# Performance work log

Hardware: AMD Instinct MI355X
Metric: run time of the kernel (lower is better)

## Reference

```python
import jax, jax.numpy as jnp
import numpy as np

B, N, D, H, DH, F, L, LC = 32, 256, 512, 8, 64, 2048, 8, 2
NEG = -1e9
SCALE = 1.0 / float(np.sqrt(DH))


def _ln(x, g, b, eps=1e-3):
    # keras LayerNormalization default epsilon=1e-3
    m = jnp.mean(x, -1, keepdims=True)
    v = jnp.mean((x - m) ** 2, -1, keepdims=True)
    return (x - m) * jax.lax.rsqrt(v + eps) * g + b


def setup_inputs() -> dict:
    key = jax.random.key(0)
    ks = jax.random.split(key, 20)
    n = lambda k, s: jax.random.normal(k, s, dtype=jnp.float32) * 0.02
    lengths = jax.random.randint(ks[0], (B,), N // 2, N + 1)
    mask = jnp.arange(N)[None, :] < lengths[:, None]  # [B,N] bool
    return {
        'x': jax.random.normal(ks[1], (B, N, D), dtype=jnp.float32),
        'interaction': jax.random.normal(ks[2], (B, N, N, H), dtype=jnp.float32) * 0.1,
        'class_token': n(ks[3], (1, 1, D)),
        'p_ln1_g': jnp.ones((L, D)), 'p_ln1_b': jnp.zeros((L, D)),
        'p_wq': n(ks[4], (L, D, D)), 'p_wk': n(ks[5], (L, D, D)),
        'p_wv': n(ks[6], (L, D, D)), 'p_wo': n(ks[7], (L, D, D)),
        'p_ln2_g': jnp.ones((L, D)), 'p_ln2_b': jnp.zeros((L, D)),
        'p_w1': n(ks[8], (L, D, F)), 'p_b1': jnp.zeros((L, F)),
        'p_w2': n(ks[9], (L, F, D)), 'p_b2': jnp.zeros((L, D)),
        'c_ln1_g': jnp.ones((LC, D)), 'c_ln1_b': jnp.zeros((LC, D)),
        'c_qk': n(ks[10], (LC, D, H, DH)), 'c_qb': jnp.zeros((LC, H, DH)),
        'c_kk': n(ks[11], (LC, D, H, DH)), 'c_kb': jnp.zeros((LC, H, DH)),
        'c_vk': n(ks[12], (LC, D, H, DH)), 'c_vb': jnp.zeros((LC, H, DH)),
        'c_ok': n(ks[13], (LC, H, DH, D)), 'c_ob': jnp.zeros((LC, D)),
        'c_ln2_g': jnp.ones((LC, D)), 'c_ln2_b': jnp.zeros((LC, D)),
        'c_w1': n(ks[14], (LC, D, F)), 'c_b1': jnp.zeros((LC, F)),
        'c_w2': n(ks[15], (LC, F, D)), 'c_b2': jnp.zeros((LC, D)),
        'mask': mask,
    }


def _part_forward(x, interaction, class_token, p_ln1_g, p_ln1_b, p_wq, p_wk, p_wv, p_wo,
                  p_ln2_g, p_ln2_b, p_w1, p_b1, p_w2, p_b2,
                  c_ln1_g, c_ln1_b, c_qk, c_qb, c_kk, c_kb, c_vk, c_vb, c_ok, c_ob,
                  c_ln2_g, c_ln2_b, c_w1, c_b1, c_w2, c_b2, mask):
    # pairwise particle mask [B,1,N,N]; keras Softmax adds (1-mask)*-1e9
    pmask = (mask[:, None, None, :] & mask[:, None, :, None]).astype(x.dtype)
    padd = (1.0 - pmask) * NEG
    inter = jnp.transpose(interaction, (0, 3, 1, 2))  # [B,H,N,N]
    h = x
    for i in range(L):
        # pre-LN interaction self-attention (dropout inactive at inference)
        hn = _ln(h, p_ln1_g[i], p_ln1_b[i])
        q = (hn @ p_wq[i]).reshape(B, N, H, DH)
        k = (hn @ p_wk[i]).reshape(B, N, H, DH)
        v = (hn @ p_wv[i]).reshape(B, N, H, DH)
        s = jnp.einsum('bqhd,bkhd->bhqk', q, k) * SCALE + inter + padd
        a = jax.nn.softmax(s, axis=-1)
        o = jnp.einsum('bhqk,bkhd->bqhd', a, v).reshape(B, N, D) @ p_wo[i]
        h = h + o
        # pre-LN FFN, gelu (exact, tf.nn.gelu default)
        fn = _ln(h, p_ln2_g[i], p_ln2_b[i])
        h = h + (jax.nn.gelu(fn @ p_w1[i] + p_b1[i], approximate=False) @ p_w2[i] + p_b2[i])
    query = jnp.broadcast_to(class_token, (B, 1, D)).astype(x.dtype)
    cmask = jnp.concatenate([jnp.ones((B, 1), bool), mask], axis=1)[:, None, None, :].astype(x.dtype)
    cadd = (1.0 - cmask) * NEG  # [B,1,1,N+1]
    for i in range(LC):
        # class-attention: K/V from LN(concat([token, particles])), Q from RAW token (as in source)
        cat = jnp.concatenate([query, h], axis=1)  # [B,N+1,D]
        cn = _ln(cat, c_ln1_g[i], c_ln1_b[i])
        qh = jnp.einsum('bqd,dhk->bqhk', query, c_qk[i]) + c_qb[i]
        kh = jnp.einsum('bsd,dhk->bshk', cn, c_kk[i]) + c_kb[i]
        vh = jnp.einsum('bsd,dhk->bshk', cn, c_vk[i]) + c_vb[i]
        s = jnp.einsum('bqhk,bshk->bhqs', qh, kh) * SCALE + cadd
        a = jax.nn.softmax(s, axis=-1)
        o = jnp.einsum('bhqs,bshk->bqhk', a, vh)
        o = jnp.einsum('bqhk,hkd->bqd', o, c_ok[i]) + c_ob[i]
        query = query + o
        fn = _ln(query, c_ln2_g[i], c_ln2_b[i])
        query = query + (jax.nn.gelu(fn @ c_w1[i] + c_b1[i], approximate=False) @ c_w2[i] + c_b2[i])
    return query  # [B,1,D]


def reference(x, interaction, class_token, p_ln1_g, p_ln1_b, p_wq, p_wk, p_wv, p_wo,
              p_ln2_g, p_ln2_b, p_w1, p_b1, p_w2, p_b2,
              c_ln1_g, c_ln1_b, c_qk, c_qb, c_kk, c_kb, c_vk, c_vb, c_ok, c_ob,
              c_ln2_g, c_ln2_b, c_w1, c_b1, c_w2, c_b2, mask):
    return _part_forward(x, interaction, class_token, p_ln1_g, p_ln1_b, p_wq, p_wk, p_wv, p_wo,
                         p_ln2_g, p_ln2_b, p_w1, p_b1, p_w2, p_b2,
                         c_ln1_g, c_ln1_b, c_qk, c_qb, c_kk, c_kb, c_vk, c_vb, c_ok, c_ob,
                         c_ln2_g, c_ln2_b, c_w1, c_b1, c_w2, c_b2, mask)
```

## Files before the change

### kernel.cpp

```cpp
#include <hip/hip_runtime.h>
#include <hip/hip_fp16.h>

#define B_ 32
#define N_ 256
#define D_ 512
#define H_ 8
#define DH_ 64
#define F_ 2048
#define L_ 8
#define LC_ 2
#define NEG_ (-1e9f)
#define SCALE_ 0.125f
#define LDSK 72
#define KCH_ 128

typedef unsigned short u16;
typedef unsigned int u32;
typedef long long s64;
typedef __attribute__((ext_vector_type(8))) short bf16x8;
typedef __attribute__((ext_vector_type(8))) unsigned short u16x8;
typedef __attribute__((ext_vector_type(4))) float f32x4;

__device__ __forceinline__ float b2f(u16 u) {
    union { u32 i; float f; } v; v.i = ((u32)u) << 16; return v.f;
}
__device__ __forceinline__ u16 f2b(float f) {
    union { float f; u32 i; } v; v.f = f;
    u32 x = v.i;
    u32 r = (x + 0x7FFFu + ((x >> 16) & 1u)) >> 16;
    return (u16)r;
}
__device__ __forceinline__ float h2f(u16 u) {
    __half_raw hr; hr.x = u;
    return __half2float(__half(hr));
}
__device__ __forceinline__ void gld16(u16* lds, const u16* g) {
    __builtin_amdgcn_global_load_lds(
        (const __attribute__((address_space(1))) u16*)g,
        (__attribute__((address_space(3))) u16*)lds, 16, 0, 0);
}
__device__ __forceinline__ float ldf(const void* p, size_t i, int fl) {
    if (fl == 1) return ((const float*)p)[i];
    if (fl == 0) return b2f(((const u16*)p)[i]);
    return h2f(((const u16*)p)[i]);
}
__device__ __forceinline__ void ld4(const void* p, size_t i, int fl, float o[4]) {
    if (fl == 1) {
        const float4 v = *(const float4*)((const float*)p + i);
        o[0] = v.x; o[1] = v.y; o[2] = v.z; o[3] = v.w;
    } else if (fl == 0) {
        const ushort4 v = *(const ushort4*)((const u16*)p + i);
        o[0] = b2f(v.x); o[1] = b2f(v.y); o[2] = b2f(v.z); o[3] = b2f(v.w);
    } else {
        const ushort4 v = *(const ushort4*)((const u16*)p + i);
        o[0] = h2f(v.x); o[1] = h2f(v.y); o[2] = h2f(v.z); o[3] = h2f(v.w);
    }
}

__global__ void sniff_kernel(const u32* __restrict__ g1, int* __restrict__ flag) {
    if (threadIdx.x == 0 && blockIdx.x == 0) {
        u32 w = g1[0];
        int f = 0;
        if (w == 0x3F800000u) f = 1;
        else if (w == 0x3C003C00u) f = 2;
        flag[0] = f;
    }
}

__global__ void mask_decode_kernel(const unsigned char* __restrict__ raw,
                                   float* __restrict__ mf) {
    int i = blockIdx.x * 256 + threadIdx.x;
    if (i >= B_ * N_) return;
    unsigned char c0 = raw[0], c1 = raw[1], c4 = raw[4];
    bool v;
    if (c1 == 0x3F || c1 == 0x3C) {
        v = ((const u16*)raw)[i] != 0;
    } else if (c0 == 1 && c1 == 1) {
        v = raw[i] != 0;
    } else if (c0 == 1 && c1 == 0) {
        if (c4 == 1) v = ((const int*)raw)[i] != 0;
        else v = ((const long long*)raw)[i] != 0;
    } else {
        v = ((const float*)raw)[i] != 0.0f;
    }
    mf[i] = v ? 1.0f : 0.0f;
}

__global__ void cvt_in_kernel(const void* __restrict__ in, float* __restrict__ out,
                              int n, const int* __restrict__ fl) {
    int i = blockIdx.x * 256 + threadIdx.x;
    if (i < n) out[i] = ldf(in, (size_t)i, fl[0]);
}
__global__ void bcast_token_kernel(const void* __restrict__ ct, float* __restrict__ qry,
                                   const int* __restrict__ fl) {
    int i = blockIdx.x * 256 + threadIdx.x;
    qry[i] = ldf(ct, (size_t)(i & (D_ - 1)), fl[0]);
}
__global__ void out_copy_kernel(const float* __restrict__ in, float* __restrict__ out, int n) {
    int i = blockIdx.x * 256 + threadIdx.x;
    if (i < n) out[i] = in[i];
}
__global__ void concat_bias_kernel(const void* __restrict__ b1, s64 o1,
                                   const void* __restrict__ b2, s64 o2,
                                   float* __restrict__ dst, const int* __restrict__ flp) {
    int i = blockIdx.x * 256 + threadIdx.x;
    if (i < 512) dst[i] = ldf(b1, (size_t)(o1 + i), flp[0]);
    else if (i < 1024) dst[i] = ldf(b2, (size_t)(o2 + i - 512), flp[0]);
}

__global__ __launch_bounds__(256) void inter_t_kernel(const void* __restrict__ inter,
                                                      const float* __restrict__ mf,
                                                      u16* __restrict__ out,
                                                      const int* __restrict__ flp) {
    __shared__ float tile[256][9];
    __shared__ float mks[256];
    int fl = flp[0];
    int bq = blockIdx.x;
    int b = bq >> 8, q = bq & 255;
    int t = threadIdx.x;
    size_t base = (size_t)bq * 2048;
#pragma unroll
    for (int p = 0; p < 8; ++p) {
        int e = p * 256 + t;
        tile[e >> 3][e & 7] = ldf(inter, base + e, fl);
    }
    mks[t] = mf[b * 256 + t];
    __syncthreads();
    float mq = mf[b * 256 + q];
    int h = t >> 5;
    int k0 = (t & 31) * 8;
    u16x8 v8;
#pragma unroll
    for (int ii = 0; ii < 8; ++ii) {
        int k = k0 + ii;
        float v = tile[k][h];
        if (mq * mks[k] < 0.5f) v += NEG_;
        v8[ii] = (short)f2b(v);
    }
    *(u16x8*)(out + (((size_t)(b * 8 + h) * 256 + q) * 256 + k0)) = v8;
}

__global__ __launch_bounds__(256) void transpose_w_kernel(const void* __restrict__ W, s64 weoff,
                                                          int Nst, int Kd,
                                                          u16* __restrict__ wt,
                                                          const int* __restrict__ flp) {
    __shared__ float tile[32][33];
    int fl = flp[0];
    int n0 = blockIdx.x * 32, k0 = blockIdx.y * 32;
    int tr = threadIdx.x >> 5, tc = threadIdx.x & 31;
#pragma unroll
    for (int p = 0; p < 4; ++p) {
        int kk = p * 8 + tr;
        tile[kk][tc] = ldf(W, (size_t)(weoff + (s64)(k0 + kk) * Nst + n0 + tc), fl);
    }
    __syncthreads();
#pragma unroll
    for (int p = 0; p < 4; ++p) {
        int nn = p * 8 + tr;
        wt[(s64)(n0 + nn) * Kd + k0 + tc] = f2b(tile[tc][nn]);
    }
}

__global__ __launch_bounds__(256) void twt6_kernel(const void* __restrict__ wq,
                                                   const void* __restrict__ wk,
                                                   const void* __restrict__ wv,
                                                   const void* __restrict__ wo,
                                                   const void* __restrict__ w1,
                                                   const void* __restrict__ w2,
                                                   s64 off44, s64 offw1, s64 offw2,
                                                   u16* __restrict__ wtqkv,
                                                   u16* __restrict__ wto,
                                                   u16* __restrict__ wt1,
                                                   u16* __restrict__ wt2,
                                                   const int* __restrict__ flp) {
    __shared__ float tile[32][33];
    int fl = flp[0];
    int bid = blockIdx.x;
    const void* W; s64 weoff; int Nst, Kd; u16* dst; int lb;
    if (bid < 256)       { W = wq; weoff = off44; Nst = 512;  Kd = 512;  dst = wtqkv;          lb = bid; }
    else if (bid < 512)  { W = wk; weoff = off44; Nst = 512;  Kd = 512;  dst = wtqkv + 262144; lb = bid - 256; }
    else if (bid < 768)  { W = wv; weoff = off44; Nst = 512;  Kd = 512;  dst = wtqkv + 524288; lb = bid - 512; }
    else if (bid < 1024) { W = wo; weoff = off44; Nst = 512;  Kd = 512;  dst = wto;            lb = bid - 768; }
    else if (bid < 2048) { W = w1; weoff = offw1; Nst = 2048; Kd = 512;  dst = wt1;            lb = bid - 1024; }
    else                 { W = w2; weoff = offw2; Nst = 512;  Kd = 2048; dst = wt2;            lb = bid - 2048; }
    int nx = Nst >> 5;
    int n0 = (lb % nx) << 5, k0 = (lb / nx) << 5;
    int tr = threadIdx.x >> 5, tc = threadIdx.x & 31;
#pragma unroll
    for (int p = 0; p < 4; ++p) {
        int kk = p * 8 + tr;
        tile[kk][tc] = ldf(W, (size_t)(weoff + (s64)(k0 + kk) * Nst + n0 + tc), fl);
    }
    __syncthreads();
#pragma unroll
    for (int p = 0; p < 4; ++p) {
        int nn = p * 8 + tr;
        dst[(s64)(n0 + nn) * Kd + k0 + tc] = f2b(tile[tc][nn]);
    }
}

__global__ __launch_bounds__(256) void ln_kernel(const float* __restrict__ in,
                                                 const void* __restrict__ g,
                                                 const void* __restrict__ bta,
                                                 s64 peoff,
                                                 u16* __restrict__ out,
                                                 const int* __restrict__ flp) {
    __shared__ float ws4[4];
    __shared__ float wsq[4];
    int fl = flp[0];
    size_t row = blockIdx.x;
    int t = threadIdx.x;
    float x0 = in[row * D_ + t];
    float x1 = in[row * D_ + 256 + t];
    float s = x0 + x1;
#pragma unroll
    for (int off = 32; off > 0; off >>= 1) s += __shfl_xor(s, off);
    if ((t & 63) == 0) ws4[t >> 6] = s;
    __syncthreads();
    float mean = (ws4[0] + ws4[1] + ws4[2] + ws4[3]) * (1.0f / D_);
    float d0 = x0 - mean, d1 = x1 - mean;
    float sq = d0 * d0 + d1 * d1;
#pragma unroll
    for (int off = 32; off > 0; off >>= 1) sq += __shfl_xor(sq, off);
    if ((t & 63) == 0) wsq[t >> 6] = sq;
    __syncthreads();
    float var = (wsq[0] + wsq[1] + wsq[2] + wsq[3]) * (1.0f / D_);
    float inv = 1.0f / sqrtf(var + 1e-3f);
    out[row * D_ + t]       = f2b(d0 * inv * ldf(g, peoff + t, fl)       + ldf(bta, peoff + t, fl));
    out[row * D_ + 256 + t] = f2b(d1 * inv * ldf(g, peoff + 256 + t, fl) + ldf(bta, peoff + 256 + t, fl));
}

__global__ __launch_bounds__(256) void ln_cat_kernel(const float* __restrict__ qry,
                                                     const float* __restrict__ h,
                                                     const void* __restrict__ g,
                                                     const void* __restrict__ bta,
                                                     s64 peoff,
                                                     u16* __restrict__ out,
                                                     const int* __restrict__ flp) {
    __shared__ float ws4[4];
    __shared__ float wsq[4];
    int fl = flp[0];
    size_t row = blockIdx.x;
    int b = (int)(row / 257);
    int r = (int)(row % 257);
    const float* src = (r == 0) ? (qry + (size_t)b * D_)
                                : (h + ((size_t)b * N_ + (r - 1)) * D_);
    int t = threadIdx.x;
    float x0 = src[t];
    float x1 = src[256 + t];
    float s = x0 + x1;
#pragma unroll
    for (int off = 32; off > 0; off >>= 1) s += __shfl_xor(s, off);
    if ((t & 63) == 0) ws4[t >> 6] = s;
    __syncthreads();
    float mean = (ws4[0] + ws4[1] + ws4[2] + ws4[3]) * (1.0f / D_);
    float d0 = x0 - mean, d1 = x1 - mean;
    float sq = d0 * d0 + d1 * d1;
#pragma unroll
    for (int off = 32; off > 0; off >>= 1) sq += __shfl_xor(sq, off);
    if ((t & 63) == 0) wsq[t >> 6] = sq;
    __syncthreads();
    float var = (wsq[0] + wsq[1] + wsq[2] + wsq[3]) * (1.0f / D_);
    float inv = 1.0f / sqrtf(var + 1e-3f);
    out[row * D_ + t]       = f2b(d0 * inv * ldf(g, peoff + t, fl)       + ldf(bta, peoff + t, fl));
    out[row * D_ + 256 + t] = f2b(d1 * inv * ldf(g, peoff + 256 + t, fl) + ldf(bta, peoff + 256 + t, fl));
}

__global__ __launch_bounds__(512) void mfma_gemm_t(const u16* __restrict__ A,
                                                   const u16* __restrict__ Wt,
                                                   int wst, int wkoff,
                                                   const void* __restrict__ bias, s64 beoff,
                                                   int bflag,
                                                   const float* __restrict__ res,
                                                   void* __restrict__ C, int cbf,
                                                   int M, int N, int K, int act,
                                                   const int* __restrict__ flp) {
    __shared__ u16 Alds[4 * 128 * 32];
    __shared__ u16 Blds[4 * 128 * 32];
    int tid = threadIdx.x;
    int gx = gridDim.x;
    int nwg = gx * gridDim.y;
    int orig = blockIdx.y * gx + blockIdx.x;
    int xcd = orig & 7;
    int qq = nwg >> 3, rr = nwg & 7;
    int wg = (xcd < rr ? xcd * (qq + 1) : rr * (qq + 1) + (xcd - rr) * qq) + (orig >> 3);
    int bx = wg % gx, by = wg / gx;
    int bm = by << 7, bn = bx << 7;
    int wid = tid >> 6, lane = tid & 63;
    int wm = (wid >> 2) << 6, wn = (wid & 3) << 5;
    int l15 = lane & 15, q = lane >> 4;
    f32x4 acc[4][2];
#pragma unroll
    for (int a = 0; a < 4; ++a)
#pragma unroll
        for (int b = 0; b < 2; ++b) acc[a][b] = (f32x4){0.f, 0.f, 0.f, 0.f};
    int srow = tid >> 2;
    int sseg = tid & 3;
    int xseg = sseg ^ (srow & 3);
    int gr = bm + srow; if (gr >= M) gr = M - 1;
    const u16* arow = A + (size_t)gr * K + (xseg << 3);
    const u16* brow = Wt + (size_t)(bn + srow) * wst + wkoff + (xseg << 3);
    int dstoff = srow * 32 + (sseg << 3);
    auto stage = [&](int buf, int k0) {
        gld16(&Alds[buf * 4096 + dstoff], arow + k0);
        gld16(&Blds[buf * 4096 + dstoff], brow + k0);
    };
    int nt = K >> 5;
    stage(0, 0);
    stage(1, 32);
    stage(2, 64);
    int sg = (q ^ (l15 & 3)) << 3;
    for (int t = 0; t < nt; ++t) {
        int rem = nt - 1 - t;
        if (rem >= 2)      asm volatile("s_waitcnt vmcnt(4)" ::: "memory");
        else if (rem == 1) asm volatile("s_waitcnt vmcnt(2)" ::: "memory");
        else               asm volatile("s_waitcnt vmcnt(0)" ::: "memory");
        __builtin_amdgcn_s_barrier();
        __builtin_amdgcn_sched_barrier(0);
        if (t + 3 < nt) stage((t + 3) & 3, (t + 3) << 5);
        const u16* Ac = Alds + (t & 3) * 4096;
        const u16* Bc = Blds + (t & 3) * 4096;
        bf16x8 af[4], bfr[2];
#pragma unroll
        for (int mt = 0; mt < 4; ++mt)
            af[mt] = *(const bf16x8*)(&Ac[(wm + mt * 16 + l15) * 32 + sg]);
#pragma unroll
        for (int nt2 = 0; nt2 < 2; ++nt2)
            bfr[nt2] = *(const bf16x8*)(&Bc[(wn + nt2 * 16 + l15) * 32 + sg]);
#pragma unroll
        for (int mt = 0; mt < 4; ++mt)
#pragma unroll
            for (int nt2 = 0; nt2 < 2; ++nt2)
                acc[mt][nt2] = __builtin_amdgcn_mfma_f32_16x16x32_bf16(
                    af[mt], bfr[nt2], acc[mt][nt2], 0, 0, 0);
        __builtin_amdgcn_sched_barrier(0);
    }
    int fl = (bflag >= 0) ? bflag : flp[0];
#pragma unroll
    for (int nt2 = 0; nt2 < 2; ++nt2) {
        int col = bn + wn + nt2 * 16 + l15;
        float bv = bias ? ldf(bias, (size_t)(beoff + col), fl) : 0.f;
#pragma unroll
        for (int mt = 0; mt < 4; ++mt) {
#pragma unroll
            for (int i = 0; i < 4; ++i) {
                int row = bm + wm + mt * 16 + q * 4 + i;
                if (row >= M) continue;
                float c = acc[mt][nt2][i] + bv;
                if (act) c = 0.5f * c * (1.0f + erff(c * 0.70710678118654752f));
                if (res) c += res[(size_t)row * N + col];
                if (cbf) ((u16*)C)[(size_t)row * N + col] = f2b(c);
                else     ((float*)C)[(size_t)row * N + col] = c;
            }
        }
    }
}

__global__ __launch_bounds__(256) void skinny_gemm_kernel(const void* __restrict__ A, int abf,
                                                          const void* __restrict__ W, s64 weoff,
                                                          int wst,
                                                          float* __restrict__ Cp,
                                                          int N, int K,
                                                          const int* __restrict__ flp) {
    __shared__ float As[32 * KCH_];
    int wfl = flp[0];
    int tid = threadIdx.x;
    int bn = blockIdx.x << 6;
    int ks = blockIdx.y;
    int k0 = ks * KCH_;
#pragma unroll
    for (int p = 0; p < (32 * KCH_) / 1024; ++p) {
        int idx = p * 1024 + tid * 4;
        int m = idx >> 7, c = idx & (KCH_ - 1);
        size_t gi = (size_t)m * K + k0 + c;
        if (abf) {
            const ushort4 v = *(const ushort4*)((const u16*)A + gi);
            As[idx]     = b2f(v.x);
            As[idx + 1] = b2f(v.y);
            As[idx + 2] = b2f(v.z);
            As[idx + 3] = b2f(v.w);
        } else {
            *(float4*)&As[idx] = *(const float4*)((const float*)A + gi);
        }
    }
    __syncthreads();
    int tx = tid & 63, ty = tid >> 6;
    int n = bn + tx;
    float acc[8] = {0.f, 0.f, 0.f, 0.f, 0.f, 0.f, 0.f, 0.f};
#pragma unroll 4
    for (int kk = 0; kk < KCH_; kk += 4) {
        float w0 = ldf(W, (size_t)(weoff + (s64)(k0 + kk) * wst + n), wfl);
        float w1 = ldf(W, (size_t)(weoff + (s64)(k0 + kk + 1) * wst + n), wfl);
        float w2 = ldf(W, (size_t)(weoff + (s64)(k0 + kk + 2) * wst + n), wfl);
        float w3 = ldf(W, (size_t)(weoff + (s64)(k0 + kk + 3) * wst + n), wfl);
#pragma unroll
        for (int r = 0; r < 8; ++r) {
            const float4 a = *(const float4*)&As[(ty * 8 + r) * KCH_ + kk];
            acc[r] += a.x * w0 + a.y * w1 + a.z * w2 + a.w * w3;
        }
    }
#pragma unroll
    for (int r = 0; r < 8; ++r)
        Cp[((size_t)ks * 32 + ty * 8 + r) * N + n] = acc[r];
}

__global__ __launch_bounds__(256) void skinny_epi_kernel(const float* __restrict__ Cp,
                                                         int KS, int N,
                                                         const void* __restrict__ bias, s64 beoff,
                                                         const float* __restrict__ res,
                                                         float* __restrict__ C, int act,
                                                         const int* __restrict__ flp) {
    int i = blockIdx.x * 256 + threadIdx.x;
    if (i >= 32 * N) return;
    int n = i % N;
    float s = 0.f;
    for (int ks = 0; ks < KS; ++ks) s += Cp[(size_t)ks * 32 * N + i];
    if (bias) s += ldf(bias, (size_t)(beoff + n), flp[0]);
    if (act) s = 0.5f * s * (1.0f + erff(s * 0.70710678118654752f));
    if (res) s += res[i];
    C[i] = s;
}

__global__ __launch_bounds__(256) void attn_mfma_kernel(const u16* __restrict__ QKV,
                                                        const u16* __restrict__ IT,
                                                        u16* __restrict__ O) {
    __shared__ u16 KV[256 * 72];
    __shared__ u16 Amat[64 * 264];
    int li = blockIdx.y * 4 + blockIdx.x;
    int slot = li >> 3;
    int bh = (li & 7) * 32 + (slot >> 2);
    int q0 = (slot & 3) << 6;
    int b = bh >> 3, hh = bh & 7;
    int tid = threadIdx.x;
    int w = tid >> 6, l = tid & 63, q2 = l >> 4, l15 = l & 15;
    int qrow = q0 + (w << 4) + l15;
    const u16* qptr = QKV + (size_t)(b * N_ + qrow) * 1536 + hh * DH_ + (q2 << 3);
    bf16x8 aq0 = *(const bf16x8*)(qptr);
    bf16x8 aq1 = *(const bf16x8*)(qptr + 32);
    {
        int r = tid >> 3, seg = (tid & 7) << 3;
#pragma unroll
        for (int p = 0; p < 8; ++p) {
            int k = p * 32 + r;
            *(u16x8*)(&KV[k * LDSK + seg]) =
                *(const u16x8*)(QKV + (size_t)(b * N_ + k) * 1536 + 512 + hh * DH_ + seg);
        }
    }
    u16x8 vreg[8];
    {
        const u16* vptr = QKV + (size_t)(b * N_ + (w << 6)) * 1536 + 1024 + hh * DH_ + l;
#pragma unroll
        for (int s = 0; s < 8; ++s)
#pragma unroll
            for (int e = 0; e < 8; ++e)
                vreg[s][e] = vptr[(size_t)(s * 8 + e) * 1536];
    }
    const u16* itp = IT + ((size_t)bh * N_ + q0 + (w << 4) + (q2 << 2)) * N_ + l15;
    u16 itv0[16], itv1[16], itv2[16], itv3[16];
#pragma unroll
    for (int t = 0; t < 16; ++t) {
        itv0[t] = itp[t * 16];
        itv1[t] = itp[(size_t)N_ + t * 16];
        itv2[t] = itp[(size_t)2 * N_ + t * 16];
        itv3[t] = itp[(size_t)3 * N_ + t * 16];
    }
    asm volatile("s_waitcnt lgkmcnt(0)" ::: "memory");
    __builtin_amdgcn_s_barrier();
    __builtin_amdgcn_sched_barrier(0);
    f32x4 acc[16];
#pragma unroll
    for (int t = 0; t < 16; ++t) {
        const u16* kp = &KV[(t * 16 + l15) * LDSK + (q2 << 3)];
        bf16x8 b0 = *(const bf16x8*)(kp);
        bf16x8 b1 = *(const bf16x8*)(kp + 32);
        f32x4 z = (f32x4){0.f, 0.f, 0.f, 0.f};
        z = __builtin_amdgcn_mfma_f32_16x16x32_bf16(aq0, b0, z, 0, 0, 0);
        acc[t] = __builtin_amdgcn_mfma_f32_16x16x32_bf16(aq1, b1, z, 0, 0, 0);
    }
    asm volatile("s_waitcnt lgkmcnt(0)" ::: "memory");
    __builtin_amdgcn_s_barrier();
    __builtin_amdgcn_sched_barrier(0);
#pragma unroll
    for (int s = 0; s < 8; ++s)
        *(u16x8*)(&KV[l * 264 + (w << 6) + s * 8]) = vreg[s];
    float mx[4] = {-3e38f, -3e38f, -3e38f, -3e38f};
#pragma unroll
    for (int t = 0; t < 16; ++t) {
        float s0 = acc[t][0] * SCALE_ + b2f(itv0[t]);
        float s1 = acc[t][1] * SCALE_ + b2f(itv1[t]);
        float s2 = acc[t][2] * SCALE_ + b2f(itv2[t]);
        float s3 = acc[t][3] * SCALE_ + b2f(itv3[t]);
        acc[t][0] = s0; acc[t][1] = s1; acc[t][2] = s2; acc[t][3] = s3;
        mx[0] = fmaxf(mx[0], s0);
        mx[1] = fmaxf(mx[1], s1);
        mx[2] = fmaxf(mx[2], s2);
        mx[3] = fmaxf(mx[3], s3);
    }
#pragma unroll
    for (int i = 0; i < 4; ++i) {
        mx[i] = fmaxf(mx[i], __shfl_xor(mx[i], 1));
        mx[i] = fmaxf(mx[i], __shfl_xor(mx[i], 2));
        mx[i] = fmaxf(mx[i], __shfl_xor(mx[i], 4));
        mx[i] = fmaxf(mx[i], __shfl_xor(mx[i], 8));
    }
    float sum[4] = {0.f, 0.f, 0.f, 0.f};
#pragma unroll
    for (int t = 0; t < 16; ++t)
#pragma unroll
        for (int i = 0; i < 4; ++i) {
            float e = expf(acc[t][i] - mx[i]);
            acc[t][i] = e;
            sum[i] += e;
        }
#pragma unroll
    for (int i = 0; i < 4; ++i) {
        sum[i] += __shfl_xor(sum[i], 1);
        sum[i] += __shfl_xor(sum[i], 2);
        sum[i] += __shfl_xor(sum[i], 4);
        sum[i] += __shfl_xor(sum[i], 8);
        sum[i] = 1.0f / sum[i];
    }
#pragma unroll
    for (int t = 0; t < 16; ++t)
#pragma unroll
        for (int i = 0; i < 4; ++i)
            Amat[((w << 4) + (q2 << 2) + i) * 264 + t * 16 + l15] = f2b(acc[t][i] * sum[i]);
    asm volatile("s_waitcnt lgkmcnt(0)" ::: "memory");
    __builtin_amdgcn_s_barrier();
    __builtin_amdgcn_sched_barrier(0);
    f32x4 pacc[4];
#pragma unroll
    for (int dt = 0; dt < 4; ++dt) pacc[dt] = (f32x4){0.f, 0.f, 0.f, 0.f};
#pragma unroll
    for (int kc = 0; kc < 8; ++kc) {
        bf16x8 af = *(const bf16x8*)(&Amat[((w << 4) + l15) * 264 + kc * 32 + (q2 << 3)]);
#pragma unroll
        for (int dt = 0; dt < 4; ++dt) {
            bf16x8 bf = *(const bf16x8*)(&KV[(dt * 16 + l15) * 264 + kc * 32 + (q2 << 3)]);
            pacc[dt] = __builtin_amdgcn_mfma_f32_16x16x32_bf16(af, bf, pacc[dt], 0, 0, 0);
        }
    }
    u16* ob = O + (size_t)(b * N_ + q0 + (w << 4) + (q2 << 2)) * D_ + hh * DH_ + l15;
#pragma unroll
    for (int dt = 0; dt < 4; ++dt)
#pragma unroll
        for (int i = 0; i < 4; ++i)
            ob[(size_t)i * D_ + dt * 16] = f2b(pacc[dt][i]);
}

__global__ __launch_bounds__(256) void cls_attn_kernel(const float* __restrict__ qh,
                                                       const u16* __restrict__ kvh,
                                                       const float* __restrict__ mf,
                                                       float* __restrict__ O) {
    __shared__ float qs[64];
    __shared__ float am[257];
    __shared__ float wred[4];
    __shared__ float vred[256];
    int b = blockIdx.x >> 3, hh = blockIdx.x & 7;
    int t = threadIdx.x;
    int w = t >> 6, l = t & 63;
    if (t < 64) qs[t] = qh[(size_t)b * D_ + hh * DH_ + t];
    __syncthreads();
    const u16* krow = kvh + (size_t)(b * 257 + t) * 1024 + hh * DH_;
    float s = 0.f;
#pragma unroll
    for (int seg = 0; seg < 8; ++seg) {
        u16x8 kv8 = *(const u16x8*)(krow + seg * 8);
#pragma unroll
        for (int e = 0; e < 8; ++e) s += qs[seg * 8 + e] * b2f(kv8[e]);
    }
    float cm = (t == 0) ? 1.0f : mf[b * N_ + t - 1];
    s = s * SCALE_ + ((cm > 0.5f) ? 0.0f : NEG_);
    float s256 = -1e30f;
    if (t == 0) {
        const u16* krow2 = kvh + (size_t)(b * 257 + 256) * 1024 + hh * DH_;
        float s2 = 0.f;
#pragma unroll
        for (int seg = 0; seg < 8; ++seg) {
            u16x8 kv8 = *(const u16x8*)(krow2 + seg * 8);
#pragma unroll
            for (int e = 0; e < 8; ++e) s2 += qs[seg * 8 + e] * b2f(kv8[e]);
        }
        float cm2 = mf[b * N_ + 255];
        s256 = s2 * SCALE_ + ((cm2 > 0.5f) ? 0.0f : NEG_);
    }
    float mx = (t == 0) ? fmaxf(s, s256) : s;
#pragma unroll
    for (int off = 32; off > 0; off >>= 1) mx = fmaxf(mx, __shfl_xor(mx, off));
    if (l == 0) wred[w] = mx;
    __syncthreads();
    mx = fmaxf(fmaxf(wred[0], wred[1]), fmaxf(wred[2], wred[3]));
    float p = expf(s - mx);
    float p256 = (t == 0) ? expf(s256 - mx) : 0.f;
    float sum = p + p256;
#pragma unroll
    for (int off = 32; off > 0; off >>= 1) sum += __shfl_xor(sum, off);
    __syncthreads();
    if (l == 0) wred[w] = sum;
    __syncthreads();
    float invs = 1.0f / (wred[0] + wred[1] + wred[2] + wred[3]);
    am[t] = p * invs;
    if (t == 0) am[256] = p256 * invs;
    __syncthreads();
    int g = w, d = l;
    const u16* vcol = kvh + (size_t)(b * 257 + g * 64) * 1024 + 512 + hh * DH_ + d;
    float acc = 0.f;
#pragma unroll 8
    for (int j = 0; j < 64; ++j)
        acc += am[g * 64 + j] * b2f(vcol[(size_t)j * 1024]);
    if (g == 3)
        acc += am[256] * b2f(kvh[(size_t)(b * 257 + 256) * 1024 + 512 + hh * DH_ + d]);
    vred[t] = acc;
    __syncthreads();
    if (t < 64)
        O[(size_t)b * D_ + hh * DH_ + t] = vred[t] + vred[64 + t] + vred[128 + t] + vred[192 + t];
}

extern "C" void kernel_launch(void* const* d_in, const int* in_sizes, int n_in,
                              void* d_out, int out_size, void* d_ws, size_t ws_size,
                              hipStream_t stream) {
    const void* x           = d_in[0];
    const void* interaction = d_in[1];
    const void* class_token = d_in[2];
    const void* p_ln1_g = d_in[3];
    const void* p_ln1_b = d_in[4];
    const void* p_wq    = d_in[5];
    const void* p_wk    = d_in[6];
    const void* p_wv    = d_in[7];
    const void* p_wo    = d_in[8];
    const void* p_ln2_g = d_in[9];
    const void* p_ln2_b = d_in[10];
    const void* p_w1    = d_in[11];
    const void* p_b1    = d_in[12];
    const void* p_w2    = d_in[13];
    const void* p_b2    = d_in[14];
    const void* c_ln1_g = d_in[15];
    const void* c_ln1_b = d_in[16];
    const void* c_qk    = d_in[17];
    const void* c_qb    = d_in[18];
    const void* c_kk    = d_in[19];
    const void* c_kb    = d_in[20];
    const void* c_vk    = d_in[21];
    const void* c_vb    = d_in[22];
    const void* c_ok    = d_in[23];
    const void* c_ob    = d_in[24];
    const void* c_ln2_g = d_in[25];
    const void* c_ln2_b = d_in[26];
    const void* c_w1    = d_in[27];
    const void* c_b1    = d_in[28];
    const void* c_w2    = d_in[29];
    const void* c_b2    = d_in[30];
    const unsigned char* maskraw = (const unsigned char*)d_in[31];

    const size_t NT  = (size_t)B_ * N_;
    const size_t NTD = NT * D_;

    char* base = (char*)d_ws;
    int*   flag   = (int*)base;
    float* maskf  = (float*)(base + 64);
    float* h      = (float*)(base + 64 + 32768);
    u16*   hn     = (u16*)(h + NTD);
    u16*   qkv    = hn + (size_t)B_ * 257 * D_;
    float* qry    = (float*)(qkv + (size_t)8192 * 1536);
    float* qh     = qry + 16384;
    float* ocls   = qh + 16384;
    u16*   fnq    = (u16*)(ocls + 16384);
    float* midc   = (float*)(fnq + 16384);
    float* biaskv = midc + 65536;
    u16*   wt     = (u16*)(biaskv + 1024);
    u16*   wtqkv = wt;
    u16*   wto   = wt + 786432;
    u16*   wt1   = wt + 1048576;
    u16*   wt2   = wt + 2097152;
    u16*   inter_t = wt + 3145728;
    u16*   midfull = inter_t + (size_t)B_ * H_ * N_ * N_;
    float* cpart = (float*)(qkv + (size_t)8224 * 1024);

    auto mgemm = [&](const u16* A, const u16* Wt, int wst, int wkoff,
                     const void* bias, s64 beoff, int bflag, const float* res, void* C, int cbf,
                     int M, int N, int K, int act) {
        dim3 grid(N / 128, (M + 127) / 128);
        mfma_gemm_t<<<grid, 512, 0, stream>>>(A, Wt, wst, wkoff, bias, beoff, bflag,
                                              res, C, cbf, M, N, K, act, flag);
    };
    auto skgemm = [&](const void* A, int abf, const void* W, s64 weoff, int wst,
                      const void* bias, s64 beoff, const float* res, float* C,
                      int N, int K, int act) {
        int KS = K / KCH_;
        skinny_gemm_kernel<<<dim3(N / 64, KS), 256, 0, stream>>>(A, abf, W, weoff, wst,
                                                                 cpart, N, K, flag);
        skinny_epi_kernel<<<(32 * N + 255) / 256, 256, 0, stream>>>(cpart, KS, N, bias, beoff,
                                                                    res, C, act, flag);
    };
    auto twt = [&](const void* W, s64 weoff, int Nst, int Kd, u16* dst) {
        dim3 grid(Nst / 32, Kd / 32);
        transpose_w_kernel<<<grid, 256, 0, stream>>>(W, weoff, Nst, Kd, dst, flag);
    };

    sniff_kernel<<<1, 64, 0, stream>>>((const u32*)p_ln1_g, flag);
    mask_decode_kernel<<<32, 256, 0, stream>>>(maskraw, maskf);
    inter_t_kernel<<<8192, 256, 0, stream>>>(interaction, maskf, inter_t, flag);
    cvt_in_kernel<<<(int)(NTD / 256), 256, 0, stream>>>(x, h, (int)NTD, flag);
    bcast_token_kernel<<<64, 256, 0, stream>>>(class_token, qry, flag);

    for (int i = 0; i < L_; ++i) {
        s64 wo = (s64)i * D_ * D_;
        twt6_kernel<<<3072, 256, 0, stream>>>(p_wq, p_wk, p_wv, p_wo, p_w1, p_w2,
                                              wo, (s64)i * D_ * F_, (s64)i * F_ * D_,
                                              wtqkv, wto, wt1, wt2, flag);
        ln_kernel<<<(int)NT, 256, 0, stream>>>(h, p_ln1_g, p_ln1_b, (s64)i * D_, hn, flag);
        mgemm(hn, wtqkv, D_, 0, nullptr, 0, -1, nullptr, qkv, 1, (int)NT, 1536, D_, 0);
        attn_mfma_kernel<<<dim3(4, B_ * H_), 256, 0, stream>>>(qkv, inter_t, hn);
        mgemm(hn, wto, D_, 0, nullptr, 0, -1, h, h, 0, (int)NT, D_, D_, 0);
        ln_kernel<<<(int)NT, 256, 0, stream>>>(h, p_ln2_g, p_ln2_b, (s64)i * D_, hn, flag);
        mgemm(hn, wt1, D_, 0, p_b1, (s64)i * F_, -1, nullptr, midfull, 1,
              (int)NT, 2048, D_, 1);
        mgemm(midfull, wt2, F_, 0, p_b2, (s64)i * D_, -1, h, h, 0,
              (int)NT, D_, F_, 0);
    }

    for (int i = 0; i < LC_; ++i) {
        s64 wo = (s64)i * D_ * D_;
        twt(c_kk, wo, D_, D_, wtqkv);
        twt(c_vk, wo, D_, D_, wtqkv + 262144);
        concat_bias_kernel<<<4, 256, 0, stream>>>(c_kb, (s64)i * D_, c_vb, (s64)i * D_, biaskv, flag);
        ln_cat_kernel<<<B_ * 257, 256, 0, stream>>>(qry, h, c_ln1_g, c_ln1_b, (s64)i * D_, hn, flag);
        skgemm(qry, 0, c_qk, wo, D_, c_qb, (s64)i * D_, nullptr, qh, D_, D_, 0);
        mgemm(hn, wtqkv, D_, 0, biaskv, 0, 1, nullptr, qkv, 1, B_ * 257, 1024, D_, 0);
        cls_attn_kernel<<<B_ * H_, 256, 0, stream>>>(qh, qkv, maskf, ocls);
        skgemm(ocls, 0, c_ok, wo, D_, c_ob, (s64)i * D_, qry, qry, D_, D_, 0);
        ln_kernel<<<B_, 256, 0, stream>>>(qry, c_ln2_g, c_ln2_b, (s64)i * D_, fnq, flag);
        skgemm(fnq, 1, c_w1, (s64)i * D_ * F_, F_, c_b1, (s64)i * F_, nullptr, midc, F_, D_, 1);
        skgemm(midc, 0, c_w2, (s64)i * F_ * D_, D_, c_b2, (s64)i * D_, qry, qry, D_, F_, 0);
    }

    out_copy_kernel<<<(out_size + 255) / 256, 256, 0, stream>>>(qry, (float*)d_out, out_size);
}
```

Baseline: 2.179 ms.

## Use 256-thread GEMM with 64x64 warp tiles and triple-buffered LDS

The bf16 MFMA GEMM moves from 512 threads (8 waves, each computing a 64x32 sub-tile) to 256 threads (4 waves, each computing 64x64). Each thread now stages two rows per operand, and the LDS swizzle pattern changes to match. The LDS ring shrinks from four buffers with prefetch depth 3 to three buffers with prefetch depth 2. The aim is more MFMA reuse per LDS fragment load and less LDS footprint per block, at the cost of more accumulator registers and a shallower prefetch pipeline.

```diff
diff --git a/kernel.cpp b/kernel.cpp
--- a/kernel.cpp
+++ b/kernel.cpp
@@ -266,7 +266,7 @@
     out[row * D_ + 256 + t] = f2b(d1 * inv * ldf(g, peoff + 256 + t, fl) + ldf(bta, peoff + 256 + t, fl));
 }
 
-__global__ __launch_bounds__(512) void mfma_gemm_t(const u16* __restrict__ A,
+__global__ __launch_bounds__(256) void mfma_gemm_t(const u16* __restrict__ A,
                                                    const u16* __restrict__ Wt,
                                                    int wst, int wkoff,
                                                    const void* __restrict__ bias, s64 beoff,
@@ -275,8 +275,8 @@
                                                    void* __restrict__ C, int cbf,
                                                    int M, int N, int K, int act,
                                                    const int* __restrict__ flp) {
-    __shared__ u16 Alds[4 * 128 * 32];
-    __shared__ u16 Blds[4 * 128 * 32];
+    __shared__ u16 Alds[3 * 128 * 32];
+    __shared__ u16 Blds[3 * 128 * 32];
     int tid = threadIdx.x;
     int gx = gridDim.x;
     int nwg = gx * gridDim.y;
@@ -287,57 +287,67 @@
     int bx = wg % gx, by = wg / gx;
     int bm = by << 7, bn = bx << 7;
     int wid = tid >> 6, lane = tid & 63;
-    int wm = (wid >> 2) << 6, wn = (wid & 3) << 5;
+    int wm = (wid >> 1) << 6, wn = (wid & 1) << 6;
     int l15 = lane & 15, q = lane >> 4;
-    f32x4 acc[4][2];
+    f32x4 acc[4][4];
 #pragma unroll
     for (int a = 0; a < 4; ++a)
 #pragma unroll
-        for (int b = 0; b < 2; ++b) acc[a][b] = (f32x4){0.f, 0.f, 0.f, 0.f};
+        for (int b = 0; b < 4; ++b) acc[a][b] = (f32x4){0.f, 0.f, 0.f, 0.f};
     int srow = tid >> 2;
     int sseg = tid & 3;
-    int xseg = sseg ^ (srow & 3);
-    int gr = bm + srow; if (gr >= M) gr = M - 1;
-    const u16* arow = A + (size_t)gr * K + (xseg << 3);
-    const u16* brow = Wt + (size_t)(bn + srow) * wst + wkoff + (xseg << 3);
+    int xs0 = sseg ^ ((srow >> 2) & 3);
+    int xs1 = sseg ^ (((srow + 64) >> 2) & 3);
+    int gr0 = bm + srow;       if (gr0 >= M) gr0 = M - 1;
+    int gr1 = bm + 64 + srow;  if (gr1 >= M) gr1 = M - 1;
+    const u16* arow0 = A + (size_t)gr0 * K + (xs0 << 3);
+    const u16* arow1 = A + (size_t)gr1 * K + (xs1 << 3);
+    const u16* brow0 = Wt + (size_t)(bn + srow) * wst + wkoff + (xs0 << 3);
+    const u16* brow1 = Wt + (size_t)(bn + 64 + srow) * wst + wkoff + (xs1 << 3);
     int dstoff = srow * 32 + (sseg << 3);
     auto stage = [&](int buf, int k0) {
-        gld16(&Alds[buf * 4096 + dstoff], arow + k0);
-        gld16(&Blds[buf * 4096 + dstoff], brow + k0);
+        u16* Ab = Alds + buf * 4096;
+        u16* Bb = Blds + buf * 4096;
+        gld16(&Ab[dstoff], arow0 + k0);
+        gld16(&Ab[2048 + dstoff], arow1 + k0);
+        gld16(&Bb[dstoff], brow0 + k0);
+        gld16(&Bb[2048 + dstoff], brow1 + k0);
     };
     int nt = K >> 5;
     stage(0, 0);
     stage(1, 32);
-    stage(2, 64);
-    int sg = (q ^ (l15 & 3)) << 3;
+    int rseg = (q ^ (l15 >> 2)) << 3;
+    int rd = 0;
     for (int t = 0; t < nt; ++t) {
-        int rem = nt - 1 - t;
-        if (rem >= 2)      asm volatile("s_waitcnt vmcnt(4)" ::: "memory");
-        else if (rem == 1) asm volatile("s_waitcnt vmcnt(2)" ::: "memory");
-        else               asm volatile("s_waitcnt vmcnt(0)" ::: "memory");
+        if (t + 1 < nt) asm volatile("s_waitcnt vmcnt(4)" ::: "memory");
+        else            asm volatile("s_waitcnt vmcnt(0)" ::: "memory");
         __builtin_amdgcn_s_barrier();
         __builtin_amdgcn_sched_barrier(0);
-        if (t + 3 < nt) stage((t + 3) & 3, (t + 3) << 5);
-        const u16* Ac = Alds + (t & 3) * 4096;
-        const u16* Bc = Blds + (t & 3) * 4096;
-        bf16x8 af[4], bfr[2];
+        if (t + 2 < nt) {
+            int wr = rd + 2; if (wr >= 3) wr -= 3;
+            stage(wr, (t + 2) << 5);
+        }
+        const u16* Ac = Alds + rd * 4096;
+        const u16* Bc = Blds + rd * 4096;
+        bf16x8 af[4], bfr[4];
 #pragma unroll
         for (int mt = 0; mt < 4; ++mt)
-            af[mt] = *(const bf16x8*)(&Ac[(wm + mt * 16 + l15) * 32 + sg]);
-#pragma unroll
-        for (int nt2 = 0; nt2 < 2; ++nt2)
-            bfr[nt2] = *(const bf16x8*)(&Bc[(wn + nt2 * 16 + l15) * 32 + sg]);
+            af[mt] = *(const bf16x8*)(&Ac[(wm + mt * 16 + l15) * 32 + rseg]);
+#pragma unroll
+        for (int nt2 = 0; nt2 < 4; ++nt2)
+            bfr[nt2] = *(const bf16x8*)(&Bc[(wn + nt2 * 16 + l15) * 32 + rseg]);
 #pragma unroll
         for (int mt = 0; mt < 4; ++mt)
 #pragma unroll
-            for (int nt2 = 0; nt2 < 2; ++nt2)
+            for (int nt2 = 0; nt2 < 4; ++nt2)
                 acc[mt][nt2] = __builtin_amdgcn_mfma_f32_16x16x32_bf16(
                     af[mt], bfr[nt2], acc[mt][nt2], 0, 0, 0);
         __builtin_amdgcn_sched_barrier(0);
+        rd += 1; if (rd >= 3) rd -= 3;
     }
     int fl = (bflag >= 0) ? bflag : flp[0];
 #pragma unroll
-    for (int nt2 = 0; nt2 < 2; ++nt2) {
+    for (int nt2 = 0; nt2 < 4; ++nt2) {
         int col = bn + wn + nt2 * 16 + l15;
         float bv = bias ? ldf(bias, (size_t)(beoff + col), fl) : 0.f;
 #pragma unroll
@@ -680,7 +690,7 @@
                      const void* bias, s64 beoff, int bflag, const float* res, void* C, int cbf,
                      int M, int N, int K, int act) {
         dim3 grid(N / 128, (M + 127) / 128);
-        mfma_gemm_t<<<grid, 512, 0, stream>>>(A, Wt, wst, wkoff, bias, beoff, bflag,
+        mfma_gemm_t<<<grid, 256, 0, stream>>>(A, Wt, wst, wkoff, bias, beoff, bflag,
                                               res, C, cbf, M, N, K, act, flag);
     };
     auto skgemm = [&](const void* A, int abf, const void* W, s64 weoff, int wst,
```

Result: slower. 2.489 ms (+14.2%).
